# Performance work log

Measured on AMD Instinct MI355X. Metric: run time of the kernel, lower is better.

## Reference

```python
import jax, jax.numpy as jnp
import numpy as np

MAX_ITER = 16
TOL = 1e-3


def setup_inputs() -> dict:
    key = jax.random.key(0)
    k0, k1, k2, k3 = jax.random.split(key, 4)
    B, A, Bd, Y = 16384, 1024, 2, 128
    AT = jax.random.uniform(k0, (B, A), dtype=jnp.float32)
    K = jax.random.uniform(k1, (A, Bd), dtype=jnp.float32)
    BT = jnp.ones((Bd,), dtype=jnp.float32)  # fixed to [1, 1] in the module
    u = jax.random.uniform(k2, (A * Bd, Y), dtype=jnp.float32)
    b = jax.random.uniform(k3, (Y,), dtype=jnp.float32)
    return {"AT": AT, "K": K, "BT": BT, "u": u, "b": b}


def reference(AT, K, BT, u, b):
    batch = AT.shape[0]
    Kp = K ** 2  # 'reparam' constraint

    # Fixed-point matrix-balancing loop (torch.no_grad block) -> constants.
    Ksg = jax.lax.stop_gradient(Kp)
    ATsg = jax.lax.stop_gradient(AT)
    A_dim, B_dim = Kp.shape
    af0 = jnp.zeros((batch, A_dim), jnp.float32)
    bf0 = jnp.zeros((batch, B_dim), jnp.float32)

    def cond(carry):
        _, _, err, i = carry
        return (i < MAX_ITER) & (err >= TOL)

    def body(carry):
        af, bf, _, i = carry
        af_n = ATsg / (bf @ Ksg.T + 1.0)   # (batch, A_dim)
        bf_n = BT / (af_n @ Ksg + 1.0)     # (batch, B_dim)
        err = jnp.max(jnp.abs(af_n - af)) + jnp.max(jnp.abs(bf_n - bf))
        return af_n, bf_n, err, i + 1

    _, bf, _, _ = jax.lax.while_loop(
        cond, body, (af0, bf0, jnp.array(jnp.inf, jnp.float32), 0)
    )
    bf = jax.lax.stop_gradient(bf)

    # Final differentiable iteration.
    af = AT / (bf @ Kp.T + 1.0)            # (batch, A_dim)
    bf = BT / (af @ Kp + 1.0)              # (batch, B_dim)

    # C = K * (AF @ BF^T): rank-1 outer product per batch element.
    C = (Kp[None, :, :] * af[:, :, None] * bf[:, None, :]).reshape(batch, -1)
    return C @ u + b
```

## Files before the change

### kernel.cpp

```cpp
#include <hip/hip_runtime.h>

__device__ __forceinline__ float b2f(unsigned short h) {
    unsigned int u = ((unsigned int)h) << 16;
    return __builtin_bit_cast(float, u);
}
__device__ __forceinline__ unsigned short f2b(float f) {
    unsigned int u = __builtin_bit_cast(unsigned int, f);
    u += 0x7fffu + ((u >> 16) & 1u);
    return (unsigned short)(u >> 16);
}

typedef short bf16x8_t __attribute__((ext_vector_type(8)));
typedef float f32x4_t  __attribute__((ext_vector_type(4)));

#define LDS_PTR(p) ((__attribute__((address_space(3))) void*)(p))
#define GLB_PTR(p) ((const __attribute__((address_space(1))) void*)(p))

#define NB   16384
#define AD   1024
#define YD   128
#define ND   256

__global__ __launch_bounds__(256) void vt_kernel(
    const float* __restrict__ Kq,
    const float* __restrict__ U,
    unsigned short* __restrict__ Vt)
{
    int idx = blockIdx.x * 256 + threadIdx.x;
    int n = idx >> 10;
    int a = idx & 1023;
    int j = n >> 7;
    int y = n & 127;
    float k  = Kq[2 * a + j];
    float kp = k * k;
    float uv = U[(size_t)(2 * a + j) * YD + y];
    Vt[idx] = f2b(kp * uv);
}

__global__ __launch_bounds__(256) void row_kernel(
    const float* __restrict__ AT,
    const float* __restrict__ Kq,
    const float* __restrict__ BTv,
    unsigned short* __restrict__ afb,
    float* __restrict__ bff)
{
    int wid  = blockIdx.x * 4 + (threadIdx.x >> 6);
    int lane = threadIdx.x & 63;
    const float* at = AT + (size_t)wid * AD;

    float ta[16], kp0[16], kp1[16];
#pragma unroll
    for (int c = 0; c < 4; ++c) {
        int base = c * 256 + lane * 4;
        float4 av = *(const float4*)(at + base);
        ta[c * 4 + 0] = av.x; ta[c * 4 + 1] = av.y;
        ta[c * 4 + 2] = av.z; ta[c * 4 + 3] = av.w;
        float4 k0 = *(const float4*)(Kq + 2 * base);
        float4 k1 = *(const float4*)(Kq + 2 * base + 4);
        kp0[c * 4 + 0] = k0.x * k0.x; kp1[c * 4 + 0] = k0.y * k0.y;
        kp0[c * 4 + 1] = k0.z * k0.z; kp1[c * 4 + 1] = k0.w * k0.w;
        kp0[c * 4 + 2] = k1.x * k1.x; kp1[c * 4 + 2] = k1.y * k1.y;
        kp0[c * 4 + 3] = k1.z * k1.z; kp1[c * 4 + 3] = k1.w * k1.w;
    }

    float M[9];
#pragma unroll
    for (int i = 0; i < 9; ++i) M[i] = 0.f;
#pragma unroll
    for (int e = 0; e < 16; ++e) {
        float t = ta[e], p = kp0[e], q = kp1[e];
        float u0 = t * p, u1 = t * q;
        M[0] += u0; M[1] += u1;
        float u00 = u0 * p, u01 = u0 * q, u11 = u1 * q;
        M[2] += u00; M[3] += u01; M[4] += u11;
        M[5] += u00 * p; M[6] += u00 * q; M[7] += u01 * q; M[8] += u11 * q;
    }
#pragma unroll
    for (int i = 0; i < 9; ++i) {
        for (int m = 1; m < 64; m <<= 1) M[i] += __shfl_xor(M[i], m, 64);
    }

    float bt0 = BTv[0], bt1 = BTv[1];
    float bf0 = 0.f, bf1 = 0.f;
#pragma unroll
    for (int it = 0; it < 8; ++it) {
        float q00 = bf0 * bf0, q01 = bf0 * bf1, q11 = bf1 * bf1;
        float s0 = M[0] - (bf0 * M[2] + bf1 * M[3]) + (q00 * M[5] + 2.f * q01 * M[6] + q11 * M[7]);
        float s1 = M[1] - (bf0 * M[3] + bf1 * M[4]) + (q00 * M[6] + 2.f * q01 * M[7] + q11 * M[8]);
        bf0 = bt0 / (1.f + s0);
        bf1 = bt1 / (1.f + s1);
    }
    if (lane == 0) { bff[(size_t)wid * 2] = bf0; bff[(size_t)wid * 2 + 1] = bf1; }

    unsigned short* ao = afb + (size_t)wid * AD;
#pragma unroll
    for (int c = 0; c < 4; ++c) {
        unsigned short r[4];
#pragma unroll
        for (int e = 0; e < 4; ++e) {
            int idx = c * 4 + e;
            r[e] = f2b(ta[idx] / (1.f + bf0 * kp0[idx] + bf1 * kp1[idx]));
        }
        *(ushort4*)(ao + c * 256 + lane * 4) = make_ushort4(r[0], r[1], r[2], r[3]);
    }
}

__global__ __launch_bounds__(256) void gemm_fused_kernel(
    const unsigned short* __restrict__ Ag,
    const unsigned short* __restrict__ Bg,
    const float* __restrict__ bff,
    const float* __restrict__ bias,
    float* __restrict__ out)
{
    __shared__ __align__(16) unsigned short lA[32 * 64];
    __shared__ __align__(16) unsigned short lB[256 * 64];

    const int t = threadIdx.x;
    const int lane = t & 63;
    const int wn = t >> 6;
    const int mtile = blockIdx.x;

    f32x4_t acc[2][4];
#pragma unroll
    for (int i = 0; i < 2; ++i)
#pragma unroll
        for (int j = 0; j < 4; ++j) acc[i][j] = (f32x4_t){0.f, 0.f, 0.f, 0.f};

    const unsigned short* gA;
    const unsigned short* gB[8];
    {
        int s = t;
        int m = s >> 3;
        int c = (s & 7) ^ (m & 7);
        gA = Ag + (size_t)(mtile * 32 + m) * AD + 8 * c;
    }
#pragma unroll
    for (int i = 0; i < 8; ++i) {
        int s = i * 256 + t;
        int n = s >> 3;
        int c = (s & 7) ^ (n & 7);
        gB[i] = Bg + (size_t)n * AD + 8 * c;
    }

    for (int k0 = 0; k0 < AD; k0 += 64) {
        __builtin_amdgcn_global_load_lds(GLB_PTR(gA + k0), LDS_PTR(&lA[t * 8]), 16, 0, 0);
#pragma unroll
        for (int i = 0; i < 8; ++i)
            __builtin_amdgcn_global_load_lds(GLB_PTR(gB[i] + k0), LDS_PTR(&lB[(i * 256 + t) * 8]), 16, 0, 0);
        __syncthreads();
#pragma unroll
        for (int kk = 0; kk < 2; ++kk) {
            const int cq = kk * 4 + (lane >> 4);
            const int rr = lane & 15;
            bf16x8_t fa[2], fb[4];
#pragma unroll
            for (int i = 0; i < 2; ++i) {
                int m = i * 16 + rr;
                fa[i] = *(const bf16x8_t*)(&lA[(m * 8 + (cq ^ (m & 7))) * 8]);
            }
#pragma unroll
            for (int j = 0; j < 4; ++j) {
                int n = wn * 32 + (j & 1) * 16 + (j >> 1) * 128 + rr;
                fb[j] = *(const bf16x8_t*)(&lB[(n * 8 + (cq ^ (n & 7))) * 8]);
            }
#pragma unroll
            for (int i = 0; i < 2; ++i)
#pragma unroll
                for (int j = 0; j < 4; ++j)
                    acc[i][j] = __builtin_amdgcn_mfma_f32_16x16x32_bf16(fa[i], fb[j], acc[i][j], 0, 0, 0);
        }
        __syncthreads();
    }

    const int q = lane >> 4, col = lane & 15;
#pragma unroll
    for (int i = 0; i < 2; ++i) {
        int mbase = mtile * 32 + i * 16 + q * 4;
        float2 bfv[4];
#pragma unroll
        for (int r = 0; r < 4; ++r)
            bfv[r] = *(const float2*)(bff + (size_t)(mbase + r) * 2);
#pragma unroll
        for (int j = 0; j < 2; ++j) {
            int y = wn * 32 + j * 16 + col;
            float bv = bias[y];
#pragma unroll
            for (int r = 0; r < 4; ++r) {
                float val = bfv[r].x * acc[i][j][r] + bfv[r].y * acc[i][j + 2][r] + bv;
                out[(size_t)(mbase + r) * YD + y] = val;
            }
        }
    }
}

extern "C" void kernel_launch(void* const* d_in, const int* in_sizes, int n_in,
                              void* d_out, int out_size, void* d_ws, size_t ws_size,
                              hipStream_t stream) {
    const float* AT  = (const float*)d_in[0];
    const float* Kq  = (const float*)d_in[1];
    const float* BTv = (const float*)d_in[2];
    const float* U   = (const float*)d_in[3];
    const float* bia = (const float*)d_in[4];
    float* out = (float*)d_out;

    char* ws = (char*)d_ws;
    unsigned short* afb = (unsigned short*)(ws);
    unsigned short* Vt  = (unsigned short*)(ws + 33554432);
    float*          bff = (float*)(ws + 34078720);

    vt_kernel<<<dim3(1024), dim3(256), 0, stream>>>(Kq, U, Vt);
    row_kernel<<<dim3(NB / 4), dim3(256), 0, stream>>>(AT, Kq, BTv, afb, bff);
    gemm_fused_kernel<<<dim3(NB / 32), dim3(256), 0, stream>>>(afb, Vt, bff, bia, out);
}
```

Baseline: 134.2 us.

## Fuse row balancing into GEMM, keep activations in LDS, double-buffer B

Merges the per-row balancing kernel into the GEMM kernel. Each block now computes its 32 rows of af directly into a full-K LDS tile, and the bf scalars stay in LDS, which removes the 32 MB bf16 workspace round-trip and one kernel launch. The B (Vt) tiles are also double-buffered so the next K-slice loads while MFMAs run. In exchange each thread holds 128 AT values in registers and LDS use grows to about 128 KB per block, which forces one block per CU and can expose latency.

Measured after the change: 152.4 us. 1.14x slower.

```diff
diff --git a/kernel.cpp b/kernel.cpp
--- a/kernel.cpp
+++ b/kernel.cpp
@@ -19,7 +19,6 @@
 #define NB   16384
 #define AD   1024
 #define YD   128
-#define ND   256
 
 __global__ __launch_bounds__(256) void vt_kernel(
     const float* __restrict__ Kq,
@@ -37,117 +36,122 @@
     Vt[idx] = f2b(kp * uv);
 }
 
-__global__ __launch_bounds__(256) void row_kernel(
+__global__ __launch_bounds__(256, 1) void fused_kernel(
     const float* __restrict__ AT,
     const float* __restrict__ Kq,
     const float* __restrict__ BTv,
-    unsigned short* __restrict__ afb,
-    float* __restrict__ bff)
-{
-    int wid  = blockIdx.x * 4 + (threadIdx.x >> 6);
-    int lane = threadIdx.x & 63;
-    const float* at = AT + (size_t)wid * AD;
-
-    float ta[16], kp0[16], kp1[16];
-#pragma unroll
-    for (int c = 0; c < 4; ++c) {
-        int base = c * 256 + lane * 4;
-        float4 av = *(const float4*)(at + base);
-        ta[c * 4 + 0] = av.x; ta[c * 4 + 1] = av.y;
-        ta[c * 4 + 2] = av.z; ta[c * 4 + 3] = av.w;
-        float4 k0 = *(const float4*)(Kq + 2 * base);
-        float4 k1 = *(const float4*)(Kq + 2 * base + 4);
-        kp0[c * 4 + 0] = k0.x * k0.x; kp1[c * 4 + 0] = k0.y * k0.y;
-        kp0[c * 4 + 1] = k0.z * k0.z; kp1[c * 4 + 1] = k0.w * k0.w;
-        kp0[c * 4 + 2] = k1.x * k1.x; kp1[c * 4 + 2] = k1.y * k1.y;
-        kp0[c * 4 + 3] = k1.z * k1.z; kp1[c * 4 + 3] = k1.w * k1.w;
-    }
-
-    float M[9];
-#pragma unroll
-    for (int i = 0; i < 9; ++i) M[i] = 0.f;
-#pragma unroll
-    for (int e = 0; e < 16; ++e) {
-        float t = ta[e], p = kp0[e], q = kp1[e];
-        float u0 = t * p, u1 = t * q;
-        M[0] += u0; M[1] += u1;
-        float u00 = u0 * p, u01 = u0 * q, u11 = u1 * q;
-        M[2] += u00; M[3] += u01; M[4] += u11;
-        M[5] += u00 * p; M[6] += u00 * q; M[7] += u01 * q; M[8] += u11 * q;
-    }
-#pragma unroll
-    for (int i = 0; i < 9; ++i) {
-        for (int m = 1; m < 64; m <<= 1) M[i] += __shfl_xor(M[i], m, 64);
-    }
-
-    float bt0 = BTv[0], bt1 = BTv[1];
-    float bf0 = 0.f, bf1 = 0.f;
-#pragma unroll
-    for (int it = 0; it < 8; ++it) {
-        float q00 = bf0 * bf0, q01 = bf0 * bf1, q11 = bf1 * bf1;
-        float s0 = M[0] - (bf0 * M[2] + bf1 * M[3]) + (q00 * M[5] + 2.f * q01 * M[6] + q11 * M[7]);
-        float s1 = M[1] - (bf0 * M[3] + bf1 * M[4]) + (q00 * M[6] + 2.f * q01 * M[7] + q11 * M[8]);
-        bf0 = bt0 / (1.f + s0);
-        bf1 = bt1 / (1.f + s1);
-    }
-    if (lane == 0) { bff[(size_t)wid * 2] = bf0; bff[(size_t)wid * 2 + 1] = bf1; }
-
-    unsigned short* ao = afb + (size_t)wid * AD;
-#pragma unroll
-    for (int c = 0; c < 4; ++c) {
-        unsigned short r[4];
-#pragma unroll
-        for (int e = 0; e < 4; ++e) {
-            int idx = c * 4 + e;
-            r[e] = f2b(ta[idx] / (1.f + bf0 * kp0[idx] + bf1 * kp1[idx]));
-        }
-        *(ushort4*)(ao + c * 256 + lane * 4) = make_ushort4(r[0], r[1], r[2], r[3]);
-    }
-}
-
-__global__ __launch_bounds__(256) void gemm_fused_kernel(
-    const unsigned short* __restrict__ Ag,
-    const unsigned short* __restrict__ Bg,
-    const float* __restrict__ bff,
+    const unsigned short* __restrict__ Vt,
     const float* __restrict__ bias,
     float* __restrict__ out)
 {
-    __shared__ __align__(16) unsigned short lA[32 * 64];
-    __shared__ __align__(16) unsigned short lB[256 * 64];
-
-    const int t = threadIdx.x;
+    __shared__ __align__(16) unsigned short lA[32 * 1024];
+    __shared__ __align__(16) unsigned short lB[2][256 * 64];
+    __shared__ float lbf[32][2];
+
+    const int t    = threadIdx.x;
     const int lane = t & 63;
-    const int wn = t >> 6;
+    const int w    = t >> 6;
     const int mtile = blockIdx.x;
 
-    f32x4_t acc[2][4];
-#pragma unroll
-    for (int i = 0; i < 2; ++i)
-#pragma unroll
-        for (int j = 0; j < 4; ++j) acc[i][j] = (f32x4_t){0.f, 0.f, 0.f, 0.f};
-
-    const unsigned short* gA;
     const unsigned short* gB[8];
-    {
-        int s = t;
-        int m = s >> 3;
-        int c = (s & 7) ^ (m & 7);
-        gA = Ag + (size_t)(mtile * 32 + m) * AD + 8 * c;
-    }
 #pragma unroll
     for (int i = 0; i < 8; ++i) {
         int s = i * 256 + t;
         int n = s >> 3;
         int c = (s & 7) ^ (n & 7);
-        gB[i] = Bg + (size_t)n * AD + 8 * c;
-    }
-
+        gB[i] = Vt + (size_t)n * AD + 8 * c;
+    }
+#pragma unroll
+    for (int i = 0; i < 8; ++i)
+        __builtin_amdgcn_global_load_lds(GLB_PTR(gB[i]), LDS_PTR(&lB[0][(i * 256 + t) * 8]), 16, 0, 0);
+
+    float kp0[16], kp1[16];
+#pragma unroll
+    for (int c = 0; c < 4; ++c) {
+        int base = c * 256 + lane * 4;
+        float4 k0v = *(const float4*)(Kq + 2 * base);
+        float4 k1v = *(const float4*)(Kq + 2 * base + 4);
+        kp0[c * 4 + 0] = k0v.x * k0v.x; kp1[c * 4 + 0] = k0v.y * k0v.y;
+        kp0[c * 4 + 1] = k0v.z * k0v.z; kp1[c * 4 + 1] = k0v.w * k0v.w;
+        kp0[c * 4 + 2] = k1v.x * k1v.x; kp1[c * 4 + 2] = k1v.y * k1v.y;
+        kp0[c * 4 + 3] = k1v.z * k1v.z; kp1[c * 4 + 3] = k1v.w * k1v.w;
+    }
+    const float bt0 = BTv[0], bt1 = BTv[1];
+
+    float ta[8][16];
+    const float* atb = AT + (size_t)(mtile * 32 + w * 8) * AD;
+#pragma unroll
+    for (int r = 0; r < 8; ++r) {
+#pragma unroll
+        for (int c = 0; c < 4; ++c) {
+            float4 av = *(const float4*)(atb + (size_t)r * AD + c * 256 + lane * 4);
+            ta[r][c * 4 + 0] = av.x; ta[r][c * 4 + 1] = av.y;
+            ta[r][c * 4 + 2] = av.z; ta[r][c * 4 + 3] = av.w;
+        }
+    }
+
+#pragma unroll
+    for (int r = 0; r < 8; ++r) {
+        float M[9];
+#pragma unroll
+        for (int i2 = 0; i2 < 9; ++i2) M[i2] = 0.f;
+#pragma unroll
+        for (int e = 0; e < 16; ++e) {
+            float tv = ta[r][e], p = kp0[e], q2 = kp1[e];
+            float u0 = tv * p, u1 = tv * q2;
+            M[0] += u0; M[1] += u1;
+            float u00 = u0 * p, u01 = u0 * q2, u11 = u1 * q2;
+            M[2] += u00; M[3] += u01; M[4] += u11;
+            M[5] += u00 * p; M[6] += u00 * q2; M[7] += u01 * q2; M[8] += u11 * q2;
+        }
+#pragma unroll
+        for (int i2 = 0; i2 < 9; ++i2) {
+            for (int mm = 1; mm < 64; mm <<= 1) M[i2] += __shfl_xor(M[i2], mm, 64);
+        }
+
+        float bf0 = 0.f, bf1 = 0.f;
+#pragma unroll
+        for (int it = 0; it < 8; ++it) {
+            float q00 = bf0 * bf0, q01 = bf0 * bf1, q11 = bf1 * bf1;
+            float s0 = M[0] - (bf0 * M[2] + bf1 * M[3]) + (q00 * M[5] + 2.f * q01 * M[6] + q11 * M[7]);
+            float s1 = M[1] - (bf0 * M[3] + bf1 * M[4]) + (q00 * M[6] + 2.f * q01 * M[7] + q11 * M[8]);
+            bf0 = bt0 / (1.f + s0);
+            bf1 = bt1 / (1.f + s1);
+        }
+        const int m = w * 8 + r;
+        if (lane == 0) { lbf[m][0] = bf0; lbf[m][1] = bf1; }
+
+#pragma unroll
+        for (int c = 0; c < 4; ++c) {
+            unsigned short rr[4];
+#pragma unroll
+            for (int e = 0; e < 4; ++e) {
+                int idx = c * 4 + e;
+                rr[e] = f2b(ta[r][idx] / (1.f + bf0 * kp0[idx] + bf1 * kp1[idx]));
+            }
+            int cg = c * 4 + (lane >> 4);
+            int cl = (lane >> 1) & 7;
+            int off = (m * 128 + cg * 8 + (cl ^ (m & 7))) * 8 + (lane & 1) * 4;
+            *(ushort4*)(&lA[off]) = make_ushort4(rr[0], rr[1], rr[2], rr[3]);
+        }
+    }
+
+    __syncthreads();
+
+    f32x4_t acc[2][4];
+#pragma unroll
+    for (int i = 0; i < 2; ++i)
+#pragma unroll
+        for (int j = 0; j < 4; ++j) acc[i][j] = (f32x4_t){0.f, 0.f, 0.f, 0.f};
+
+    int buf = 0;
     for (int k0 = 0; k0 < AD; k0 += 64) {
-        __builtin_amdgcn_global_load_lds(GLB_PTR(gA + k0), LDS_PTR(&lA[t * 8]), 16, 0, 0);
-#pragma unroll
-        for (int i = 0; i < 8; ++i)
-            __builtin_amdgcn_global_load_lds(GLB_PTR(gB[i] + k0), LDS_PTR(&lB[(i * 256 + t) * 8]), 16, 0, 0);
-        __syncthreads();
+        if (k0 + 64 < AD) {
+#pragma unroll
+            for (int i = 0; i < 8; ++i)
+                __builtin_amdgcn_global_load_lds(GLB_PTR(gB[i] + k0 + 64),
+                    LDS_PTR(&lB[buf ^ 1][(i * 256 + t) * 8]), 16, 0, 0);
+        }
 #pragma unroll
         for (int kk = 0; kk < 2; ++kk) {
             const int cq = kk * 4 + (lane >> 4);
@@ -156,12 +160,12 @@
 #pragma unroll
             for (int i = 0; i < 2; ++i) {
                 int m = i * 16 + rr;
-                fa[i] = *(const bf16x8_t*)(&lA[(m * 8 + (cq ^ (m & 7))) * 8]);
+                fa[i] = *(const bf16x8_t*)(&lA[(m * 128 + (k0 >> 6) * 8 + (cq ^ (m & 7))) * 8]);
             }
 #pragma unroll
             for (int j = 0; j < 4; ++j) {
-                int n = wn * 32 + (j & 1) * 16 + (j >> 1) * 128 + rr;
-                fb[j] = *(const bf16x8_t*)(&lB[(n * 8 + (cq ^ (n & 7))) * 8]);
+                int n = w * 32 + (j & 1) * 16 + (j >> 1) * 128 + rr;
+                fb[j] = *(const bf16x8_t*)(&lB[buf][(n * 8 + (cq ^ (n & 7))) * 8]);
             }
 #pragma unroll
             for (int i = 0; i < 2; ++i)
@@ -170,19 +174,21 @@
                     acc[i][j] = __builtin_amdgcn_mfma_f32_16x16x32_bf16(fa[i], fb[j], acc[i][j], 0, 0, 0);
         }
         __syncthreads();
+        buf ^= 1;
     }
 
     const int q = lane >> 4, col = lane & 15;
 #pragma unroll
     for (int i = 0; i < 2; ++i) {
-        int mbase = mtile * 32 + i * 16 + q * 4;
+        int mloc  = i * 16 + q * 4;
+        int mbase = mtile * 32 + mloc;
         float2 bfv[4];
 #pragma unroll
         for (int r = 0; r < 4; ++r)
-            bfv[r] = *(const float2*)(bff + (size_t)(mbase + r) * 2);
+            bfv[r] = *(const float2*)(&lbf[mloc + r][0]);
 #pragma unroll
         for (int j = 0; j < 2; ++j) {
-            int y = wn * 32 + j * 16 + col;
+            int y = w * 32 + j * 16 + col;
             float bv = bias[y];
 #pragma unroll
             for (int r = 0; r < 4; ++r) {
@@ -203,12 +209,8 @@
     const float* bia = (const float*)d_in[4];
     float* out = (float*)d_out;
 
-    char* ws = (char*)d_ws;
-    unsigned short* afb = (unsigned short*)(ws);
-    unsigned short* Vt  = (unsigned short*)(ws + 33554432);
-    float*          bff = (float*)(ws + 34078720);
+    unsigned short* Vt = (unsigned short*)d_ws;
 
     vt_kernel<<<dim3(1024), dim3(256), 0, stream>>>(Kq, U, Vt);
-    row_kernel<<<dim3(NB / 4), dim3(256), 0, stream>>>(AT, Kq, BTv, afb, bff);
-    gemm_fused_kernel<<<dim3(NB / 32), dim3(256), 0, stream>>>(afb, Vt, bff, bia, out);
-}
+    fused_kernel<<<dim3(NB / 32), dim3(256), 0, stream>>>(AT, Kq, BTv, Vt, bia, out);
+}
```
